# Performance work log

Hardware: AMD Instinct MI355X
Metric: run time of the kernel (lower is better)

## Reference

```python
import jax, jax.numpy as jnp
import numpy as np

N_NODES = 50000
HIDDEN = 128
N_REL = 9
N_LAYERS = 3
N_EDGES = 600000


def setup_inputs() -> dict:
    key = jax.random.key(0)
    k1, k2, k3, k4, k5 = jax.random.split(key, 5)
    edge_index = jax.random.randint(k1, (2, N_EDGES), 0, N_NODES, dtype=jnp.int64 if jax.config.jax_enable_x64 else jnp.int32)
    edge_type = jax.random.randint(k2, (N_EDGES,), 0, N_REL, dtype=edge_index.dtype)
    embeddings = jax.random.uniform(k3, (N_NODES, HIDDEN), dtype=jnp.float32)
    weights = jax.random.uniform(k4, (N_LAYERS, N_REL, HIDDEN, HIDDEN), dtype=jnp.float32)
    biases = jax.random.uniform(k5, (N_LAYERS, N_REL, HIDDEN), dtype=jnp.float32)
    return {"edge_index": edge_index, "edge_type": edge_type,
            "embeddings": embeddings, "weights": weights, "biases": biases}


def reference(edge_index, edge_type, embeddings, weights, biases):
    # RGCN: per relation r, messages = emb[src] @ W[l,r] + b[l,r], scatter-summed
    # into dest. Equivalent vectorized form: precompute X = emb @ W for all
    # relations ([R,N,E]), then a single gather + segment_sum over edges.
    L = weights.shape[0]
    N = embeddings.shape[0]
    dest = edge_index[0]
    src = edge_index[1]
    out = embeddings
    for l in range(L):
        X = jnp.einsum('ne,ref->rnf', out, weights[l])        # [R, N, E]
        msg = X[edge_type, src] + biases[l][edge_type]        # [num_edges, E]
        hidden = jax.ops.segment_sum(msg, dest, num_segments=N)  # [N, E]
        if l + 1 < L:
            hidden = jax.nn.relu(hidden)
        out = hidden
    return out
```

## Files before the change

kernel.cpp:

```cpp
#include <hip/hip_runtime.h>

#define NNODES 50000
#define HID 128
#define NREL 9
#define NLAYERS 3
#define NEDGES 600000

#define NBINS (NREL * NNODES)
#define SCAN_CHUNK 1024
#define NBLK ((NBINS + SCAN_CHUNK - 1) / SCAN_CHUNK)

#define KTOT (NREL * HID)
#define GM2 64
#define BK 64
#define NCHUNK (KTOT / BK)
#define PITCH 72
#define EPITCH 136

#define HIST_BLKS ((NEDGES + 255) / 256)
#define EMB_BLKS  ((NNODES * HID / 8) / 256)
#define W_BLKS    (NLAYERS * NREL)

typedef __attribute__((ext_vector_type(8))) short short8;
typedef __attribute__((ext_vector_type(4))) float f32x4;

__device__ __forceinline__ short f2bf(float f) {
    union { float f; unsigned u; } c; c.f = f;
    unsigned r = c.u + 0x7fff + ((c.u >> 16) & 1);
    return (short)(r >> 16);
}
__device__ __forceinline__ float bf2f(short v) {
    return __uint_as_float(((unsigned)(unsigned short)v) << 16);
}


__global__ __launch_bounds__(256) void prep_kernel(const int* __restrict__ dst,
                                                   const int* __restrict__ etype,
                                                   int* __restrict__ bins,
                                                   const float* __restrict__ E,
                                                   short* __restrict__ Ebf,
                                                   const float* __restrict__ W,
                                                   short* __restrict__ Wt2) {
    int b = blockIdx.x, tid = threadIdx.x;
    if (b < HIST_BLKS) {
        int e = b * 256 + tid;
        if (e < NEDGES) {
            int bin = dst[e] * NREL + etype[e];
            atomicAdd(&bins[bin], 1);
        }
    } else if (b < HIST_BLKS + EMB_BLKS) {
        int gid = (b - HIST_BLKS) * 256 + tid;
        const float* p = E + (size_t)gid * 8;
        float4 v0 = *(const float4*)p;
        float4 v1 = *(const float4*)(p + 4);
        short8 o = {f2bf(v0.x), f2bf(v0.y), f2bf(v0.z), f2bf(v0.w),
                    f2bf(v1.x), f2bf(v1.y), f2bf(v1.z), f2bf(v1.w)};
        *(short8*)(Ebf + (size_t)gid * 8) = o;
    } else {
        int lr = b - HIST_BLKS - EMB_BLKS;
        int l = lr / NREL, r = lr - l * NREL;
        const float* w = W + (size_t)lr * HID * HID;
        short* o = Wt2 + (size_t)l * HID * KTOT;
#pragma unroll 4
        for (int i = 0; i < 64; i++) {
            int elem = i * 256 + tid;
            int kk = elem >> 7, n = elem & 127;
            o[(size_t)n * KTOT + r * HID + kk] = f2bf(w[elem]);
        }
    }
}


__global__ __launch_bounds__(256) void scan_pass1(const int* __restrict__ bins,
                                                  int* __restrict__ blocksum) {
    __shared__ int red[256];
    int b = blockIdx.x, t = threadIdx.x;
    int i0 = b * SCAN_CHUNK + t * 4;
    int s = 0;
#pragma unroll
    for (int k = 0; k < 4; k++)
        if (i0 + k < NBINS) s += bins[i0 + k];
    red[t] = s;
    __syncthreads();
    for (int off = 128; off > 0; off >>= 1) {
        if (t < off) red[t] += red[t + off];
        __syncthreads();
    }
    if (t == 0) blocksum[b] = red[0];
}

__global__ __launch_bounds__(512) void scan_pass2(const int* __restrict__ blocksum,
                                                  int* __restrict__ blockoff,
                                                  int* __restrict__ rowptr) {
    __shared__ int s[512];
    int t = threadIdx.x;
    int v = (t < NBLK) ? blocksum[t] : 0;
    s[t] = v;
    __syncthreads();
    for (int off = 1; off < 512; off <<= 1) {
        int x = (t >= off) ? s[t - off] : 0;
        __syncthreads();
        s[t] += x;
        __syncthreads();
    }
    if (t < NBLK) blockoff[t] = s[t] - v;
    if (t == 0) rowptr[NBINS] = NEDGES;
}

__global__ __launch_bounds__(256) void scan_pass3(const int* __restrict__ bins,
                                                  const int* __restrict__ blockoff,
                                                  int* __restrict__ rowptr,
                                                  int* __restrict__ cursor) {
    __shared__ int sc[256];
    int b = blockIdx.x, t = threadIdx.x;
    int i0 = b * SCAN_CHUNK + t * 4;
    int v[4], p[4];
    int s = 0;
#pragma unroll
    for (int k = 0; k < 4; k++) {
        v[k] = (i0 + k < NBINS) ? bins[i0 + k] : 0;
        p[k] = s;
        s += v[k];
    }
    sc[t] = s;
    __syncthreads();
    for (int off = 1; off < 256; off <<= 1) {
        int x = (t >= off) ? sc[t - off] : 0;
        __syncthreads();
        sc[t] += x;
        __syncthreads();
    }
    int base = blockoff[b] + (sc[t] - s);
#pragma unroll
    for (int k = 0; k < 4; k++) {
        if (i0 + k < NBINS) {
            rowptr[i0 + k] = base + p[k];
            cursor[i0 + k] = base + p[k];
        }
    }
}

__global__ void place_kernel(const int* __restrict__ dst, const int* __restrict__ src,
                             const int* __restrict__ etype,
                             int* __restrict__ cursor, int* __restrict__ bsrc) {
    int e = blockIdx.x * blockDim.x + threadIdx.x;
    if (e < NEDGES) {
        int bin = dst[e] * NREL + etype[e];
        int pos = atomicAdd(&cursor[bin], 1);
        bsrc[pos] = src[e];
    }
}


__global__ __launch_bounds__(256) void gather_kernel(const short* __restrict__ Hbf,
                                                     const int* __restrict__ bsrc,
                                                     const int* __restrict__ rowptr,
                                                     short* __restrict__ S) {
    int gid = blockIdx.x * blockDim.x + threadIdx.x;
    int bin = gid >> 3;
    if (bin >= NBINS) return;
    int ck  = gid & 7;
    int rs = rowptr[bin];
    int re = rowptr[bin + 1];
    float a[16];
#pragma unroll
    for (int i = 0; i < 16; i++) a[i] = 0.f;
    for (int j = rs; j < re; j++) {
        int s = bsrc[j];
        const short* hp = Hbf + (size_t)s * HID + ck * 16;
        short8 v0 = *(const short8*)hp;
        short8 v1 = *(const short8*)(hp + 8);
#pragma unroll
        for (int i = 0; i < 8; i++) a[i]     += bf2f(v0[i]);
#pragma unroll
        for (int i = 0; i < 8; i++) a[i + 8] += bf2f(v1[i]);
    }
    short8 o0 = {f2bf(a[0]),  f2bf(a[1]),  f2bf(a[2]),  f2bf(a[3]),
                 f2bf(a[4]),  f2bf(a[5]),  f2bf(a[6]),  f2bf(a[7])};
    short8 o1 = {f2bf(a[8]),  f2bf(a[9]),  f2bf(a[10]), f2bf(a[11]),
                 f2bf(a[12]), f2bf(a[13]), f2bf(a[14]), f2bf(a[15])};
    short* sp = S + (size_t)bin * HID + ck * 16;
    *(short8*)sp       = o0;
    *(short8*)(sp + 8) = o1;
}


__global__ __launch_bounds__(256) void gemm_kernel(const short* __restrict__ S,
                                                   const short* __restrict__ Wt2l,
                                                   const float* __restrict__ Bias,
                                                   const int* __restrict__ rowptr,
                                                   short* __restrict__ HoutBf,
                                                   float* __restrict__ HoutF,
                                                   int last) {
    __shared__ short lds[GM2 * PITCH + HID * PITCH];
    __shared__ int   rp_s[GM2 * NREL + 1];
    __shared__ float bias_s[NREL * HID];
    short* As = lds;
    short* Bs = lds + GM2 * PITCH;

    int tid  = threadIdx.x;
    int wave = tid >> 6, lane = tid & 63;
    int row0 = blockIdx.x * GM2;
    int m0   = wave * 16;
    int lm = lane & 15, lq = lane >> 4;

    int rpbase = row0 * NREL;
    for (int i = tid; i <= GM2 * NREL; i += 256) {
        int g = rpbase + i;
        rp_s[i] = rowptr[(g < NBINS) ? g : NBINS];
    }
    for (int i = tid; i < NREL * HID; i += 256) bias_s[i] = Bias[i];

    int rowL = tid >> 3;
    int ck   = tid & 7;
    int ar0 = row0 + rowL;        if (ar0 > NNODES - 1) ar0 = NNODES - 1;
    int ar1 = row0 + 32 + rowL;   if (ar1 > NNODES - 1) ar1 = NNODES - 1;
    const short* pA0 = S + (size_t)ar0 * KTOT + ck * 8;
    const short* pA1 = S + (size_t)ar1 * KTOT + ck * 8;
    const short* pB0 = Wt2l + (size_t)(rowL      ) * KTOT + ck * 8;
    const short* pB1 = Wt2l + (size_t)(rowL + 32 ) * KTOT + ck * 8;
    const short* pB2 = Wt2l + (size_t)(rowL + 64 ) * KTOT + ck * 8;
    const short* pB3 = Wt2l + (size_t)(rowL + 96 ) * KTOT + ck * 8;

    short8 raE0 = *(const short8*)pA0;
    short8 raE1 = *(const short8*)pA1;
    short8 raO0 = *(const short8*)(pA0 + BK);
    short8 raO1 = *(const short8*)(pA1 + BK);
    short8 rb0 = *(const short8*)pB0;
    short8 rb1 = *(const short8*)pB1;
    short8 rb2 = *(const short8*)pB2;
    short8 rb3 = *(const short8*)pB3;

    f32x4 acc[8];
#pragma unroll
    for (int nt = 0; nt < 8; nt++) acc[nt] = (f32x4){0.f, 0.f, 0.f, 0.f};

    for (int kp = 0; kp < NCHUNK / 2; kp++) {
        int ke = 2 * kp;
        __syncthreads();
        *(short8*)&As[ rowL       * PITCH + ck * 8] = raE0;
        *(short8*)&As[(rowL + 32) * PITCH + ck * 8] = raE1;
        *(short8*)&Bs[ rowL       * PITCH + ck * 8] = rb0;
        *(short8*)&Bs[(rowL + 32) * PITCH + ck * 8] = rb1;
        *(short8*)&Bs[(rowL + 64) * PITCH + ck * 8] = rb2;
        *(short8*)&Bs[(rowL + 96) * PITCH + ck * 8] = rb3;
        __syncthreads();
        if (ke + 2 < NCHUNK) {
            int off = (ke + 2) * BK;
            raE0 = *(const short8*)(pA0 + off);
            raE1 = *(const short8*)(pA1 + off);
        }
        {
            int off = (ke + 1) * BK;
            rb0 = *(const short8*)(pB0 + off);
            rb1 = *(const short8*)(pB1 + off);
            rb2 = *(const short8*)(pB2 + off);
            rb3 = *(const short8*)(pB3 + off);
        }
#pragma unroll
        for (int ks = 0; ks < 2; ks++) {
            short8 af = *(const short8*)&As[(m0 + lm) * PITCH + ks * 32 + lq * 8];
#pragma unroll
            for (int nt = 0; nt < 8; nt++) {
                short8 bf = *(const short8*)&Bs[(nt * 16 + lm) * PITCH + ks * 32 + lq * 8];
                acc[nt] = __builtin_amdgcn_mfma_f32_16x16x32_bf16(af, bf, acc[nt], 0, 0, 0);
            }
        }
        __syncthreads();
        *(short8*)&As[ rowL       * PITCH + ck * 8] = raO0;
        *(short8*)&As[(rowL + 32) * PITCH + ck * 8] = raO1;
        *(short8*)&Bs[ rowL       * PITCH + ck * 8] = rb0;
        *(short8*)&Bs[(rowL + 32) * PITCH + ck * 8] = rb1;
        *(short8*)&Bs[(rowL + 64) * PITCH + ck * 8] = rb2;
        *(short8*)&Bs[(rowL + 96) * PITCH + ck * 8] = rb3;
        __syncthreads();
        if (ke + 3 < NCHUNK) {
            int off = (ke + 3) * BK;
            raO0 = *(const short8*)(pA0 + off);
            raO1 = *(const short8*)(pA1 + off);
        }
        if (ke + 2 < NCHUNK) {
            int off = (ke + 2) * BK;
            rb0 = *(const short8*)(pB0 + off);
            rb1 = *(const short8*)(pB1 + off);
            rb2 = *(const short8*)(pB2 + off);
            rb3 = *(const short8*)(pB3 + off);
        }
#pragma unroll
        for (int ks = 0; ks < 2; ks++) {
            short8 af = *(const short8*)&As[(m0 + lm) * PITCH + ks * 32 + lq * 8];
#pragma unroll
            for (int nt = 0; nt < 8; nt++) {
                short8 bf = *(const short8*)&Bs[(nt * 16 + lm) * PITCH + ks * 32 + lq * 8];
                acc[nt] = __builtin_amdgcn_mfma_f32_16x16x32_bf16(af, bf, acc[nt], 0, 0, 0);
            }
        }
    }
    __syncthreads();

    if (!last) {
        short (*Et)[EPITCH] = (short(*)[EPITCH])lds;
#pragma unroll
        for (int reg = 0; reg < 4; reg++) {
            int rl = m0 + lq * 4 + reg;
            float cr[NREL];
#pragma unroll
            for (int r = 0; r < NREL; r++)
                cr[r] = (float)(rp_s[rl * NREL + r + 1] - rp_s[rl * NREL + r]);
#pragma unroll
            for (int nt = 0; nt < 8; nt++) {
                int n = nt * 16 + lm;
                float b = 0.f;
#pragma unroll
                for (int r = 0; r < NREL; r++) b += cr[r] * bias_s[r * HID + n];
                float o = fmaxf(acc[nt][reg] + b, 0.f);
                Et[rl][n] = f2bf(o);
            }
        }
        __syncthreads();
#pragma unroll
        for (int i = 0; i < 4; i++) {
            int p = i * 256 + tid;
            int row = p >> 4, cc = p & 15;
            int d = row0 + row;
            if (d < NNODES)
                *(short8*)(HoutBf + (size_t)d * HID + cc * 8) = *(const short8*)&Et[row][cc * 8];
        }
    } else {
#pragma unroll
        for (int reg = 0; reg < 4; reg++) {
            int rl = m0 + lq * 4 + reg;
            int d  = row0 + rl;
            if (d >= NNODES) continue;
            float cr[NREL];
#pragma unroll
            for (int r = 0; r < NREL; r++)
                cr[r] = (float)(rp_s[rl * NREL + r + 1] - rp_s[rl * NREL + r]);
#pragma unroll
            for (int nt = 0; nt < 8; nt++) {
                int n = nt * 16 + lm;
                float b = 0.f;
#pragma unroll
                for (int r = 0; r < NREL; r++) b += cr[r] * bias_s[r * HID + n];
                HoutF[(size_t)d * HID + n] = acc[nt][reg] + b;
            }
        }
    }
}


extern "C" void kernel_launch(void* const* d_in, const int* in_sizes, int n_in,
                              void* d_out, int out_size, void* d_ws, size_t ws_size,
                              hipStream_t stream) {
    const int*   edge_index = (const int*)d_in[0];
    const int*   etype      = (const int*)d_in[1];
    const float* emb        = (const float*)d_in[2];
    const float* W          = (const float*)d_in[3];
    const float* Bias       = (const float*)d_in[4];
    float*       out        = (float*)d_out;

    const int* dst  = edge_index;
    const int* srcA = edge_index + NEDGES;

    short* Ebf = (short*)d_ws;
    short* Hbf = Ebf + (size_t)NNODES * HID;
    short* S   = Hbf + (size_t)NNODES * HID;
    short* Wt2 = S + (size_t)NNODES * KTOT;
    int*   bsrc     = (int*)(Wt2 + (size_t)NLAYERS * HID * KTOT);
    int*   bins     = bsrc + NEDGES;
    int*   cursor   = bins + NBINS;
    int*   rowptr   = cursor + NBINS;
    int*   blocksum = rowptr + NBINS + 1;
    int*   blockoff = blocksum + NBLK;

    hipMemsetAsync(bins, 0, NBINS * sizeof(int), stream);
    prep_kernel<<<HIST_BLKS + EMB_BLKS + W_BLKS, 256, 0, stream>>>(
        dst, etype, bins, emb, Ebf, W, Wt2);
    scan_pass1<<<NBLK, 256, 0, stream>>>(bins, blocksum);
    scan_pass2<<<1, 512, 0, stream>>>(blocksum, blockoff, rowptr);
    scan_pass3<<<NBLK, 256, 0, stream>>>(bins, blockoff, rowptr, cursor);
    place_kernel<<<(NEDGES + 255) / 256, 256, 0, stream>>>(dst, srcA, etype, cursor, bsrc);

    const short* Hin = Ebf;
    for (int l = 0; l < NLAYERS; l++) {
        gather_kernel<<<(NBINS * 8 + 255) / 256, 256, 0, stream>>>(Hin, bsrc, rowptr, S);
        const short* Wtl = Wt2 + (size_t)l * HID * KTOT;
        const float* Bl  = Bias + (size_t)l * NREL * HID;
        int last = (l + 1 == NLAYERS);
        gemm_kernel<<<(NNODES + GM2 - 1) / GM2, 256, 0, stream>>>(
            S, Wtl, Bl, rowptr, Hbf, out, last);
        Hin = Hbf;
    }
}
```

Before: 417.3 us.

## Load GEMM weight fragments straight from global and double-buffer A tile in LDS

The GEMM kernel no longer stages the weight (B) tile through shared memory. Each wave now owns a 32-column slice of the output and loads its B fragments directly from global memory into registers, while all four row tiles of A are read from LDS. The A tile is double-buffered in LDS, which cuts the barriers per K-step from two pairs to one. This removes B LDS traffic and synchronisation, at the cost of uncoalesced per-lane global loads of the weights, which rely on L2 hits, and a different MFMA register layout.

```diff
diff --git a/kernel.cpp b/kernel.cpp
--- a/kernel.cpp
+++ b/kernel.cpp
@@ -192,16 +192,15 @@
                                                    short* __restrict__ HoutBf,
                                                    float* __restrict__ HoutF,
                                                    int last) {
-    __shared__ short lds[GM2 * PITCH + HID * PITCH];
+    __shared__ short lds[2 * GM2 * PITCH];
     __shared__ int   rp_s[GM2 * NREL + 1];
     __shared__ float bias_s[NREL * HID];
-    short* As = lds;
-    short* Bs = lds + GM2 * PITCH;
+    short* As0 = lds;
+    short* As1 = lds + GM2 * PITCH;
 
     int tid  = threadIdx.x;
     int wave = tid >> 6, lane = tid & 63;
     int row0 = blockIdx.x * GM2;
-    int m0   = wave * 16;
     int lm = lane & 15, lq = lane >> 4;
 
     int rpbase = row0 * NREL;
@@ -217,104 +216,116 @@
     int ar1 = row0 + 32 + rowL;   if (ar1 > NNODES - 1) ar1 = NNODES - 1;
     const short* pA0 = S + (size_t)ar0 * KTOT + ck * 8;
     const short* pA1 = S + (size_t)ar1 * KTOT + ck * 8;
-    const short* pB0 = Wt2l + (size_t)(rowL      ) * KTOT + ck * 8;
-    const short* pB1 = Wt2l + (size_t)(rowL + 32 ) * KTOT + ck * 8;
-    const short* pB2 = Wt2l + (size_t)(rowL + 64 ) * KTOT + ck * 8;
-    const short* pB3 = Wt2l + (size_t)(rowL + 96 ) * KTOT + ck * 8;
-
-    short8 raE0 = *(const short8*)pA0;
-    short8 raE1 = *(const short8*)pA1;
-    short8 raO0 = *(const short8*)(pA0 + BK);
-    short8 raO1 = *(const short8*)(pA1 + BK);
-    short8 rb0 = *(const short8*)pB0;
-    short8 rb1 = *(const short8*)pB1;
-    short8 rb2 = *(const short8*)pB2;
-    short8 rb3 = *(const short8*)pB3;
-
-    f32x4 acc[8];
-#pragma unroll
-    for (int nt = 0; nt < 8; nt++) acc[nt] = (f32x4){0.f, 0.f, 0.f, 0.f};
+
+    const short* wb = Wt2l + (size_t)(wave * 32 + lm) * KTOT + lq * 8;
+
+    short8 aE0 = *(const short8*)pA0;
+    short8 aE1 = *(const short8*)pA1;
+    *(short8*)&As0[ rowL       * PITCH + ck * 8] = aE0;
+    *(short8*)&As0[(rowL + 32) * PITCH + ck * 8] = aE1;
+    short8 bE[4], bO[4];
+#pragma unroll
+    for (int nt = 0; nt < 2; nt++)
+#pragma unroll
+        for (int ks = 0; ks < 2; ks++) {
+            bE[nt * 2 + ks] = *(const short8*)(wb + (size_t)nt * 16 * KTOT + 0 * BK + ks * 32);
+            bO[nt * 2 + ks] = *(const short8*)(wb + (size_t)nt * 16 * KTOT + 1 * BK + ks * 32);
+        }
+    short8 aO0 = *(const short8*)(pA0 + BK);
+    short8 aO1 = *(const short8*)(pA1 + BK);
+    aE0 = *(const short8*)(pA0 + 2 * BK);
+    aE1 = *(const short8*)(pA1 + 2 * BK);
+
+    f32x4 acc[4][2];
+#pragma unroll
+    for (int mt = 0; mt < 4; mt++)
+#pragma unroll
+        for (int nt = 0; nt < 2; nt++) acc[mt][nt] = (f32x4){0.f, 0.f, 0.f, 0.f};
+
+    __syncthreads();
 
     for (int kp = 0; kp < NCHUNK / 2; kp++) {
         int ke = 2 * kp;
-        __syncthreads();
-        *(short8*)&As[ rowL       * PITCH + ck * 8] = raE0;
-        *(short8*)&As[(rowL + 32) * PITCH + ck * 8] = raE1;
-        *(short8*)&Bs[ rowL       * PITCH + ck * 8] = rb0;
-        *(short8*)&Bs[(rowL + 32) * PITCH + ck * 8] = rb1;
-        *(short8*)&Bs[(rowL + 64) * PITCH + ck * 8] = rb2;
-        *(short8*)&Bs[(rowL + 96) * PITCH + ck * 8] = rb3;
-        __syncthreads();
+#pragma unroll
+        for (int ks = 0; ks < 2; ks++) {
+            short8 af0 = *(const short8*)&As0[(lm     ) * PITCH + ks * 32 + lq * 8];
+            short8 af1 = *(const short8*)&As0[(lm + 16) * PITCH + ks * 32 + lq * 8];
+            short8 af2 = *(const short8*)&As0[(lm + 32) * PITCH + ks * 32 + lq * 8];
+            short8 af3 = *(const short8*)&As0[(lm + 48) * PITCH + ks * 32 + lq * 8];
+#pragma unroll
+            for (int nt = 0; nt < 2; nt++) {
+                acc[0][nt] = __builtin_amdgcn_mfma_f32_16x16x32_bf16(af0, bE[nt * 2 + ks], acc[0][nt], 0, 0, 0);
+                acc[1][nt] = __builtin_amdgcn_mfma_f32_16x16x32_bf16(af1, bE[nt * 2 + ks], acc[1][nt], 0, 0, 0);
+                acc[2][nt] = __builtin_amdgcn_mfma_f32_16x16x32_bf16(af2, bE[nt * 2 + ks], acc[2][nt], 0, 0, 0);
+                acc[3][nt] = __builtin_amdgcn_mfma_f32_16x16x32_bf16(af3, bE[nt * 2 + ks], acc[3][nt], 0, 0, 0);
+            }
+        }
+        *(short8*)&As1[ rowL       * PITCH + ck * 8] = aO0;
+        *(short8*)&As1[(rowL + 32) * PITCH + ck * 8] = aO1;
+        if (ke + 3 < NCHUNK) {
+            aO0 = *(const short8*)(pA0 + (ke + 3) * BK);
+            aO1 = *(const short8*)(pA1 + (ke + 3) * BK);
+        }
         if (ke + 2 < NCHUNK) {
-            int off = (ke + 2) * BK;
-            raE0 = *(const short8*)(pA0 + off);
-            raE1 = *(const short8*)(pA1 + off);
-        }
-        {
-            int off = (ke + 1) * BK;
-            rb0 = *(const short8*)(pB0 + off);
-            rb1 = *(const short8*)(pB1 + off);
-            rb2 = *(const short8*)(pB2 + off);
-            rb3 = *(const short8*)(pB3 + off);
-        }
+#pragma unroll
+            for (int nt = 0; nt < 2; nt++)
+#pragma unroll
+                for (int ks = 0; ks < 2; ks++)
+                    bE[nt * 2 + ks] = *(const short8*)(wb + (size_t)nt * 16 * KTOT + (ke + 2) * BK + ks * 32);
+        }
+        __syncthreads();
 #pragma unroll
         for (int ks = 0; ks < 2; ks++) {
-            short8 af = *(const short8*)&As[(m0 + lm) * PITCH + ks * 32 + lq * 8];
-#pragma unroll
-            for (int nt = 0; nt < 8; nt++) {
-                short8 bf = *(const short8*)&Bs[(nt * 16 + lm) * PITCH + ks * 32 + lq * 8];
-                acc[nt] = __builtin_amdgcn_mfma_f32_16x16x32_bf16(af, bf, acc[nt], 0, 0, 0);
+            short8 af0 = *(const short8*)&As1[(lm     ) * PITCH + ks * 32 + lq * 8];
+            short8 af1 = *(const short8*)&As1[(lm + 16) * PITCH + ks * 32 + lq * 8];
+            short8 af2 = *(const short8*)&As1[(lm + 32) * PITCH + ks * 32 + lq * 8];
+            short8 af3 = *(const short8*)&As1[(lm + 48) * PITCH + ks * 32 + lq * 8];
+#pragma unroll
+            for (int nt = 0; nt < 2; nt++) {
+                acc[0][nt] = __builtin_amdgcn_mfma_f32_16x16x32_bf16(af0, bO[nt * 2 + ks], acc[0][nt], 0, 0, 0);
+                acc[1][nt] = __builtin_amdgcn_mfma_f32_16x16x32_bf16(af1, bO[nt * 2 + ks], acc[1][nt], 0, 0, 0);
+                acc[2][nt] = __builtin_amdgcn_mfma_f32_16x16x32_bf16(af2, bO[nt * 2 + ks], acc[2][nt], 0, 0, 0);
+                acc[3][nt] = __builtin_amdgcn_mfma_f32_16x16x32_bf16(af3, bO[nt * 2 + ks], acc[3][nt], 0, 0, 0);
             }
         }
-        __syncthreads();
-        *(short8*)&As[ rowL       * PITCH + ck * 8] = raO0;
-        *(short8*)&As[(rowL + 32) * PITCH + ck * 8] = raO1;
-        *(short8*)&Bs[ rowL       * PITCH + ck * 8] = rb0;
-        *(short8*)&Bs[(rowL + 32) * PITCH + ck * 8] = rb1;
-        *(short8*)&Bs[(rowL + 64) * PITCH + ck * 8] = rb2;
-        *(short8*)&Bs[(rowL + 96) * PITCH + ck * 8] = rb3;
-        __syncthreads();
+        if (ke + 2 < NCHUNK) {
+            *(short8*)&As0[ rowL       * PITCH + ck * 8] = aE0;
+            *(short8*)&As0[(rowL + 32) * PITCH + ck * 8] = aE1;
+        }
+        if (ke + 4 < NCHUNK) {
+            aE0 = *(const short8*)(pA0 + (ke + 4) * BK);
+            aE1 = *(const short8*)(pA1 + (ke + 4) * BK);
+        }
         if (ke + 3 < NCHUNK) {
-            int off = (ke + 3) * BK;
-            raO0 = *(const short8*)(pA0 + off);
-            raO1 = *(const short8*)(pA1 + off);
-        }
-        if (ke + 2 < NCHUNK) {
-            int off = (ke + 2) * BK;
-            rb0 = *(const short8*)(pB0 + off);
-            rb1 = *(const short8*)(pB1 + off);
-            rb2 = *(const short8*)(pB2 + off);
-            rb3 = *(const short8*)(pB3 + off);
-        }
-#pragma unroll
-        for (int ks = 0; ks < 2; ks++) {
-            short8 af = *(const short8*)&As[(m0 + lm) * PITCH + ks * 32 + lq * 8];
-#pragma unroll
-            for (int nt = 0; nt < 8; nt++) {
-                short8 bf = *(const short8*)&Bs[(nt * 16 + lm) * PITCH + ks * 32 + lq * 8];
-                acc[nt] = __builtin_amdgcn_mfma_f32_16x16x32_bf16(af, bf, acc[nt], 0, 0, 0);
-            }
-        }
-    }
-    __syncthreads();
+#pragma unroll
+            for (int nt = 0; nt < 2; nt++)
+#pragma unroll
+                for (int ks = 0; ks < 2; ks++)
+                    bO[nt * 2 + ks] = *(const short8*)(wb + (size_t)nt * 16 * KTOT + (ke + 3) * BK + ks * 32);
+        }
+        __syncthreads();
+    }
 
     if (!last) {
         short (*Et)[EPITCH] = (short(*)[EPITCH])lds;
 #pragma unroll
-        for (int reg = 0; reg < 4; reg++) {
-            int rl = m0 + lq * 4 + reg;
-            float cr[NREL];
-#pragma unroll
-            for (int r = 0; r < NREL; r++)
-                cr[r] = (float)(rp_s[rl * NREL + r + 1] - rp_s[rl * NREL + r]);
-#pragma unroll
-            for (int nt = 0; nt < 8; nt++) {
-                int n = nt * 16 + lm;
-                float b = 0.f;
-#pragma unroll
-                for (int r = 0; r < NREL; r++) b += cr[r] * bias_s[r * HID + n];
-                float o = fmaxf(acc[nt][reg] + b, 0.f);
-                Et[rl][n] = f2bf(o);
+        for (int mt = 0; mt < 4; mt++) {
+#pragma unroll
+            for (int reg = 0; reg < 4; reg++) {
+                int rl = mt * 16 + lq * 4 + reg;
+                float cr[NREL];
+#pragma unroll
+                for (int r = 0; r < NREL; r++)
+                    cr[r] = (float)(rp_s[rl * NREL + r + 1] - rp_s[rl * NREL + r]);
+#pragma unroll
+                for (int nt = 0; nt < 2; nt++) {
+                    int n = wave * 32 + nt * 16 + lm;
+                    float b = 0.f;
+#pragma unroll
+                    for (int r = 0; r < NREL; r++) b += cr[r] * bias_s[r * HID + n];
+                    float o = fmaxf(acc[mt][nt][reg] + b, 0.f);
+                    Et[rl][n] = f2bf(o);
+                }
             }
         }
         __syncthreads();
@@ -328,21 +339,24 @@
         }
     } else {
 #pragma unroll
-        for (int reg = 0; reg < 4; reg++) {
-            int rl = m0 + lq * 4 + reg;
-            int d  = row0 + rl;
-            if (d >= NNODES) continue;
-            float cr[NREL];
-#pragma unroll
-            for (int r = 0; r < NREL; r++)
-                cr[r] = (float)(rp_s[rl * NREL + r + 1] - rp_s[rl * NREL + r]);
-#pragma unroll
-            for (int nt = 0; nt < 8; nt++) {
-                int n = nt * 16 + lm;
-                float b = 0.f;
-#pragma unroll
-                for (int r = 0; r < NREL; r++) b += cr[r] * bias_s[r * HID + n];
-                HoutF[(size_t)d * HID + n] = acc[nt][reg] + b;
+        for (int mt = 0; mt < 4; mt++) {
+#pragma unroll
+            for (int reg = 0; reg < 4; reg++) {
+                int rl = mt * 16 + lq * 4 + reg;
+                int d  = row0 + rl;
+                if (d >= NNODES) continue;
+                float cr[NREL];
+#pragma unroll
+                for (int r = 0; r < NREL; r++)
+                    cr[r] = (float)(rp_s[rl * NREL + r + 1] - rp_s[rl * NREL + r]);
+#pragma unroll
+                for (int nt = 0; nt < 2; nt++) {
+                    int n = wave * 32 + nt * 16 + lm;
+                    float b = 0.f;
+#pragma unroll
+                    for (int r = 0; r < NREL; r++) b += cr[r] * bias_s[r * HID + n];
+                    HoutF[(size_t)d * HID + n] = acc[mt][nt][reg] + b;
+                }
             }
         }
     }
```

Result: no change. 422.8 us (+1.3%).
